# Optimization experiments

Measured on AMD Instinct MI355X. Metric: run time of the kernel, lower is better.

## Reference

```python
import jax, jax.numpy as jnp
import numpy as np

B, NPG, DEG, F, H, C = 256, 256, 16, 128, 128, 10
N = B * NPG
E = N * DEG
RATIO = 0.5
K1 = int(np.ceil(RATIO * NPG))       # 128
K2 = int(np.ceil(RATIO * K1))        # 64
K3 = int(np.ceil(RATIO * K2))        # 32


def _glorot(key, shape):
    lim = np.sqrt(6.0 / (shape[0] + shape[1]))
    return jax.random.uniform(key, shape, jnp.float32, -lim, lim)


def setup_inputs() -> dict:
    key = jax.random.key(0)
    ks = jax.random.split(key, 16)
    x = jax.random.normal(ks[0], (N, F), jnp.float32)
    epg = E // B
    g = jnp.repeat(jnp.arange(B, dtype=jnp.int32), epg)
    src = jax.random.randint(ks[1], (E,), 0, NPG, jnp.int32) + g * NPG
    dst = jax.random.randint(ks[2], (E,), 0, NPG, jnp.int32) + g * NPG
    edge_index = jnp.stack([src, dst])
    batch = jnp.repeat(jnp.arange(B, dtype=jnp.int32), NPG)
    return {
        "x": x, "edge_index": edge_index, "batch": batch,
        "W1": _glorot(ks[3], (F, H)), "b1": jnp.zeros((H,), jnp.float32),
        "Wp1": _glorot(ks[4], (H, 1)), "bp1": jnp.zeros((1,), jnp.float32),
        "W2": _glorot(ks[5], (H, H)), "b2": jnp.zeros((H,), jnp.float32),
        "Wp2": _glorot(ks[6], (H, 1)), "bp2": jnp.zeros((1,), jnp.float32),
        "W3": _glorot(ks[7], (H, H)), "b3": jnp.zeros((H,), jnp.float32),
        "Wp3": _glorot(ks[8], (H, 1)), "bp3": jnp.zeros((1,), jnp.float32),
        "Wl1": _glorot(ks[9], (2 * H, H)), "bl1": jnp.zeros((H,), jnp.float32),
        "Wl2": _glorot(ks[10], (H, H // 2)), "bl2": jnp.zeros((H // 2,), jnp.float32),
        "Wl3": _glorot(ks[11], (H // 2, C)), "bl3": jnp.zeros((C,), jnp.float32),
    }


def gcn_conv(x, src, dst, emask, nmask, W, b):
    # PyG GCNConv: symmetric normalization with self-loops, edge weights = emask.
    h = x @ W
    deg = jax.ops.segment_sum(emask, dst, num_segments=N) + nmask  # self-loop on active nodes
    dinv = jnp.where(deg > 0, jax.lax.rsqrt(deg), 0.0)
    w = emask * dinv[src] * dinv[dst]                      # [E]
    agg = jax.ops.segment_sum(h[src] * w[:, None], dst, num_segments=N)
    out = agg + h * (dinv * dinv * nmask)[:, None] + b
    return out * nmask[:, None]


def topk_pool(x, src, dst, emask, nmask, Wp, bp, k):
    # SAGPool-style gcn_pool: score via GCNConv(H->1), per-graph top-k,
    # x <- x * tanh(score) on kept nodes, edges restricted to kept nodes.
    s = gcn_conv(x, src, dst, emask, nmask, Wp, bp)[:, 0]   # [N]
    sm = jnp.where(nmask > 0, s, -jnp.inf).reshape(B, NPG)
    idx = jax.lax.top_k(sm, k)[1]                           # [B,k]
    newmask = jnp.zeros((B, NPG), x.dtype).at[jnp.arange(B)[:, None], idx].set(1.0).reshape(-1)
    x_new = x * jnp.tanh(s)[:, None] * newmask[:, None]
    emask_new = emask * newmask[src] * newmask[dst]
    return x_new, emask_new, newmask


def readout(x, nmask, batch):
    # cat([global_max_pool, global_mean_pool]) over remaining nodes per graph
    cnt = jax.ops.segment_sum(nmask, batch, num_segments=B)
    mean = jax.ops.segment_sum(x, batch, num_segments=B) / cnt[:, None]
    xinf = jnp.where(nmask[:, None] > 0, x, -jnp.inf)
    mx = jax.ops.segment_max(xinf, batch, num_segments=B)
    return jnp.concatenate([mx, mean], axis=1)


def reference(x, edge_index, batch, W1, b1, Wp1, bp1, W2, b2, Wp2, bp2, W3, b3, Wp3, bp3,
              Wl1, bl1, Wl2, bl2, Wl3, bl3):
    src, dst = edge_index[0], edge_index[1]
    emask = jnp.ones((E,), x.dtype)
    nmask = jnp.ones((N,), x.dtype)

    h = jax.nn.relu(gcn_conv(x, src, dst, emask, nmask, W1, b1))
    h, emask, nmask = topk_pool(h, src, dst, emask, nmask, Wp1, bp1, K1)
    x1 = readout(h, nmask, batch)

    h = jax.nn.relu(gcn_conv(h, src, dst, emask, nmask, W2, b2))
    h, emask, nmask = topk_pool(h, src, dst, emask, nmask, Wp2, bp2, K2)
    x2 = readout(h, nmask, batch)

    h = jax.nn.relu(gcn_conv(h, src, dst, emask, nmask, W3, b3))
    h, emask, nmask = topk_pool(h, src, dst, emask, nmask, Wp3, bp3, K3)
    x3 = readout(h, nmask, batch)

    z = x1 + x2 + x3
    z = jax.nn.relu(z @ Wl1 + bl1)   # dropout is identity in eval mode
    z = jax.nn.relu(z @ Wl2 + bl2)
    return jax.nn.log_softmax(z @ Wl3 + bl3, axis=-1)
```

## Files before the change

kernel.cpp:

```cpp
#include <hip/hip_runtime.h>
#include <math.h>

#define NB   256
#define NPG  256
#define NN   (NB * NPG)
#define NE   (NN * 16)
#define EPG  (NE / NB)
#define FD   128
#define NC   10
#define NSL  32
#define NEG_INF (-3.402823466e38f)

struct SM {
    float hs[NPG][FD];
    int   rp[NPG + 4];
    float nmloc[NPG];
    float dvv[NPG];
    float sw[NPG];
    float sf[NPG];
    float svv[NPG];
    float th[NPG];
    float zacc[2 * FD];
    int   si[NPG];
    int   kept[NPG];
    int   anode[NPG];
    float red_mx[16][FD];
    float red_sm[16][FD];
    unsigned char colb[EPG];
};

__device__ __forceinline__ float4& hsq(SM& sm, int v, int q) {
    return *(float4*)&sm.hs[v][(q ^ (v & 7)) << 2];
}

template <int NACT>
__device__ __forceinline__ void do_level(SM& sm,
                                         const float* __restrict__ Wmat,
                                         const float* __restrict__ bias,
                                         const float* __restrict__ Wp,
                                         const float* __restrict__ bpp,
                                         int tid) {
    constexpr int NPS = NACT / NSL;
    constexpr int K   = NACT / 2;
    constexpr int TPN = 1024 / NACT;
    const int f4 = tid & 31;
    const int s  = tid >> 5;

    {
        const int n = tid >> 2, sub = tid & 3;
        float part = 0.f;
        const float nmn = sm.nmloc[n];
        if (nmn > 0.f) {
            const int e1 = sm.rp[n + 1];
            for (int e = sm.rp[n] + sub; e < e1; e += 4)
                part += sm.nmloc[sm.colb[e]];
        }
        part += __shfl_xor(part, 1);
        part += __shfl_xor(part, 2);
        if (sub == 0)
            sm.dvv[n] = (nmn > 0.f) ? rsqrtf(1.f + part) : 0.f;
    }

    {
        int vr[NPS];
        float4 acc[NPS];
#pragma unroll
        for (int c = 0; c < NPS; ++c) {
            vr[c] = sm.anode[c * NSL + s];
            acc[c] = make_float4(0.f, 0.f, 0.f, 0.f);
        }
#pragma unroll 2
        for (int kq = 0; kq < 32; ++kq) {
            const int k0 = kq << 2;
            float4 w0 = *(const float4*)&Wmat[(k0 + 0) * FD + 4 * f4];
            float4 w1 = *(const float4*)&Wmat[(k0 + 1) * FD + 4 * f4];
            float4 w2 = *(const float4*)&Wmat[(k0 + 2) * FD + 4 * f4];
            float4 w3 = *(const float4*)&Wmat[(k0 + 3) * FD + 4 * f4];
#pragma unroll
            for (int c = 0; c < NPS; ++c) {
                float4 hv = hsq(sm, vr[c], kq);
                acc[c].x += hv.x * w0.x + hv.y * w1.x + hv.z * w2.x + hv.w * w3.x;
                acc[c].y += hv.x * w0.y + hv.y * w1.y + hv.z * w2.y + hv.w * w3.y;
                acc[c].z += hv.x * w0.z + hv.y * w1.z + hv.z * w2.z + hv.w * w3.z;
                acc[c].w += hv.x * w0.w + hv.y * w1.w + hv.z * w2.w + hv.w * w3.w;
            }
        }
#pragma unroll
        for (int c = 0; c < NPS; ++c)
            hsq(sm, vr[c], f4) = acc[c];
    }
    __syncthreads();

    const float4 b4  = *(const float4*)&bias[4 * f4];
    const float4 wp4 = *(const float4*)&Wp[4 * f4];
    float4 hreg[NPS];
#pragma unroll
    for (int c = 0; c < NPS; ++c) {
        const int v = sm.anode[c * NSL + s];
        const float dv_ = sm.dvv[v], dv2 = dv_ * dv_;
        const float4 hv = hsq(sm, v, f4);
        float4 acc;
        acc.x = hv.x * dv2 + b4.x;
        acc.y = hv.y * dv2 + b4.y;
        acc.z = hv.z * dv2 + b4.z;
        acc.w = hv.w * dv2 + b4.w;
        const int e0 = sm.rp[v], e1 = sm.rp[v + 1];
        int e = e0;
        for (; e + 4 <= e1; e += 4) {
            int u0 = sm.colb[e],     u1 = sm.colb[e + 1];
            int u2 = sm.colb[e + 2], u3 = sm.colb[e + 3];
            float w0 = sm.dvv[u0] * dv_, w1 = sm.dvv[u1] * dv_;
            float w2 = sm.dvv[u2] * dv_, w3 = sm.dvv[u3] * dv_;
            float4 h0 = hsq(sm, u0, f4);
            float4 h1 = hsq(sm, u1, f4);
            float4 h2 = hsq(sm, u2, f4);
            float4 h3 = hsq(sm, u3, f4);
            acc.x += w0 * h0.x + w1 * h1.x + w2 * h2.x + w3 * h3.x;
            acc.y += w0 * h0.y + w1 * h1.y + w2 * h2.y + w3 * h3.y;
            acc.z += w0 * h0.z + w1 * h1.z + w2 * h2.z + w3 * h3.z;
            acc.w += w0 * h0.w + w1 * h1.w + w2 * h2.w + w3 * h3.w;
        }
        for (; e < e1; ++e) {
            int u = sm.colb[e];
            float w = sm.dvv[u] * dv_;
            float4 hu = hsq(sm, u, f4);
            acc.x += w * hu.x; acc.y += w * hu.y;
            acc.z += w * hu.z; acc.w += w * hu.w;
        }
        acc.x = fmaxf(acc.x, 0.f);
        acc.y = fmaxf(acc.y, 0.f);
        acc.z = fmaxf(acc.z, 0.f);
        acc.w = fmaxf(acc.w, 0.f);
        hreg[c] = acc;
        float p = acc.x * wp4.x + acc.y * wp4.y + acc.z * wp4.z + acc.w * wp4.w;
        p += __shfl_xor(p, 1);
        p += __shfl_xor(p, 2);
        p += __shfl_xor(p, 4);
        p += __shfl_xor(p, 8);
        p += __shfl_xor(p, 16);
        if (f4 == 0) sm.sw[v] = p;
    }
    __syncthreads();

    {
        const int i = tid / TPN, sub = tid % TPN;
        const int v = sm.anode[i];
        const float dv_ = sm.dvv[v];
        float part = 0.f;
        const int e1 = sm.rp[v + 1];
        for (int e = sm.rp[v] + sub; e < e1; e += TPN) {
            int u = sm.colb[e];
            part += sm.dvv[u] * sm.sw[u];
        }
#pragma unroll
        for (int o = 1; o < TPN; o <<= 1) part += __shfl_xor(part, o);
        if (sub == 0) {
            float acc = sm.sw[v] * dv_ * dv_ + bpp[0] + dv_ * part;
            sm.sf[v] = acc;
            sm.svv[i] = acc;
        }
    }
    __syncthreads();

    float v_ = 0.f;
    int   id_ = 0;
    if (tid < NACT) { v_ = sm.svv[tid]; id_ = sm.anode[tid]; }
#pragma unroll
    for (int k = 2; k <= NACT; k <<= 1) {
#pragma unroll
        for (int j = k >> 1; j > 0; j >>= 1) {
            if (j < 64) {
                if (tid < NACT) {
                    float vp = __shfl_xor(v_, j);
                    int  idp = __shfl_xor(id_, j);
                    bool up    = ((tid & k) == 0);
                    bool lower = ((tid & j) == 0);
                    bool g = (v_ > vp) || (v_ == vp && id_ < idp);
                    if (g != (lower == up)) { v_ = vp; id_ = idp; }
                }
            } else {
                if (tid < NACT) { sm.svv[tid] = v_; sm.si[tid] = id_; }
                __syncthreads();
                if (tid < NACT) {
                    int p = tid ^ j;
                    float vp = sm.svv[p];
                    int  idp = sm.si[p];
                    bool up    = ((tid & k) == 0);
                    bool lower = ((tid & j) == 0);
                    bool g = (v_ > vp) || (v_ == vp && id_ < idp);
                    if (g != (lower == up)) { v_ = vp; id_ = idp; }
                }
                __syncthreads();
            }
        }
    }
    if (tid < NPG) sm.kept[tid] = 0;
    __syncthreads();
    if (tid < K) {
        sm.kept[id_] = 1;
        sm.th[id_] = tanhf(sm.sf[id_]);
    }
    __syncthreads();

    float4 mx4 = make_float4(NEG_INF, NEG_INF, NEG_INF, NEG_INF);
    float4 sm4 = make_float4(0.f, 0.f, 0.f, 0.f);
#pragma unroll
    for (int c = 0; c < NPS; ++c) {
        const int v = sm.anode[c * NSL + s];
        if (sm.kept[v]) {
            const float tg = sm.th[v];
            float4 val;
            val.x = hreg[c].x * tg;
            val.y = hreg[c].y * tg;
            val.z = hreg[c].z * tg;
            val.w = hreg[c].w * tg;
            hsq(sm, v, f4) = val;
            mx4.x = fmaxf(mx4.x, val.x); sm4.x += val.x;
            mx4.y = fmaxf(mx4.y, val.y); sm4.y += val.y;
            mx4.z = fmaxf(mx4.z, val.z); sm4.z += val.z;
            mx4.w = fmaxf(mx4.w, val.w); sm4.w += val.w;
        }
    }
    mx4.x = fmaxf(mx4.x, __shfl_xor(mx4.x, 32)); sm4.x += __shfl_xor(sm4.x, 32);
    mx4.y = fmaxf(mx4.y, __shfl_xor(mx4.y, 32)); sm4.y += __shfl_xor(sm4.y, 32);
    mx4.z = fmaxf(mx4.z, __shfl_xor(mx4.z, 32)); sm4.z += __shfl_xor(sm4.z, 32);
    mx4.w = fmaxf(mx4.w, __shfl_xor(mx4.w, 32)); sm4.w += __shfl_xor(sm4.w, 32);
    const int wv = tid >> 6;
    if ((tid & 63) < 32) {
        *(float4*)&sm.red_mx[wv][4 * f4] = mx4;
        *(float4*)&sm.red_sm[wv][4 * f4] = sm4;
    }
    __syncthreads();
    if (tid < FD) {
        float mx = NEG_INF, smv = 0.f;
#pragma unroll
        for (int i = 0; i < 16; ++i) {
            mx = fmaxf(mx, sm.red_mx[i][tid]);
            smv += sm.red_sm[i][tid];
        }
        sm.zacc[tid] += mx;
        sm.zacc[FD + tid] += smv / (float)K;
    }
    if (tid < NPG) sm.nmloc[tid] = (float)sm.kept[tid];
    if (tid < K) sm.anode[tid] = id_;
    __syncthreads();
}

__global__ __launch_bounds__(1024)
void k_mega(const float* __restrict__ x, const int* __restrict__ ei,
            const float* __restrict__ W1, const float* __restrict__ b1,
            const float* __restrict__ Wp1, const float* __restrict__ bp1,
            const float* __restrict__ W2, const float* __restrict__ b2,
            const float* __restrict__ Wp2, const float* __restrict__ bp2,
            const float* __restrict__ W3, const float* __restrict__ b3,
            const float* __restrict__ Wp3, const float* __restrict__ bp3,
            const float* __restrict__ Wl1, const float* __restrict__ bl1,
            const float* __restrict__ Wl2, const float* __restrict__ bl2,
            const float* __restrict__ Wl3, const float* __restrict__ bl3,
            float* __restrict__ out) {
    __shared__ SM sm;
    const int g = blockIdx.x, tid = threadIdx.x;
    const int gbase = g * NPG, ebase = g * EPG;
    const int* __restrict__ srcA = ei;
    const int* __restrict__ dstA = ei + NE;

    int myd[4], mys[4];
#pragma unroll
    for (int i = 0; i < 4; ++i) {
        int e = ebase + tid + i * 1024;
        myd[i] = dstA[e] - gbase;
        mys[i] = srcA[e] - gbase;
    }

    if (tid < NPG) sm.si[tid] = 0;
    __syncthreads();
#pragma unroll
    for (int i = 0; i < 4; ++i) atomicAdd(&sm.si[myd[i]], 1);
    __syncthreads();
    if (tid < NPG) sm.anode[tid] = sm.si[tid];
    __syncthreads();
    for (int o = 1; o < NPG; o <<= 1) {
        int add = 0;
        if (tid < NPG && tid >= o) add = sm.anode[tid - o];
        __syncthreads();
        if (tid < NPG) sm.anode[tid] += add;
        __syncthreads();
    }
    if (tid < NPG) {
        int excl = sm.anode[tid] - sm.si[tid];
        sm.rp[tid] = excl;
        sm.kept[tid] = excl;
        if (tid == 0) sm.rp[NPG] = EPG;
    }
    __syncthreads();
#pragma unroll
    for (int i = 0; i < 4; ++i) {
        int p = atomicAdd(&sm.kept[myd[i]], 1);
        sm.colb[p] = (unsigned char)mys[i];
    }

    {
        const int r0 = tid >> 5, f4 = tid & 31;
        for (int r = r0; r < NPG; r += NSL)
            hsq(sm, r, f4) =
                *(const float4*)&x[((size_t)(gbase + r)) * FD + 4 * f4];
    }
    if (tid < NPG) { sm.anode[tid] = tid; sm.nmloc[tid] = 1.f; }
    if (tid < 2 * FD) sm.zacc[tid] = 0.f;
    __syncthreads();

    do_level<256>(sm, W1, b1, Wp1, bp1, tid);
    do_level<128>(sm, W2, b2, Wp2, bp2, tid);
    do_level<64>(sm, W3, b3, Wp3, bp3, tid);

    if (tid < 128) {
        float a = bl1[tid];
#pragma unroll 8
        for (int k = 0; k < 256; ++k) a += sm.zacc[k] * Wl1[k * 128 + tid];
        sm.sw[tid] = fmaxf(a, 0.f);
    }
    __syncthreads();
    if (tid < 64) {
        float a = bl2[tid];
#pragma unroll 8
        for (int k = 0; k < 128; ++k) a += sm.sw[k] * Wl2[k * 64 + tid];
        sm.sf[tid] = fmaxf(a, 0.f);
    }
    __syncthreads();
    if (tid < NC) {
        float a = bl3[tid];
#pragma unroll
        for (int k = 0; k < 64; ++k) a += sm.sf[k] * Wl3[k * NC + tid];
        sm.svv[tid] = a;
    }
    __syncthreads();
    if (tid == 0) {
        float m = sm.svv[0];
        for (int c = 1; c < NC; ++c) m = fmaxf(m, sm.svv[c]);
        float se = 0.f;
        for (int c = 0; c < NC; ++c) se += expf(sm.svv[c] - m);
        float lse = m + logf(se);
        for (int c = 0; c < NC; ++c) out[g * NC + c] = sm.svv[c] - lse;
    }
}

extern "C" void kernel_launch(void* const* d_in, const int* in_sizes, int n_in,
                              void* d_out, int out_size, void* d_ws, size_t ws_size,
                              hipStream_t stream) {
    const float* x   = (const float*)d_in[0];
    const int*   ei  = (const int*)d_in[1];
    const float* W1  = (const float*)d_in[3];
    const float* b1  = (const float*)d_in[4];
    const float* Wp1 = (const float*)d_in[5];
    const float* bp1 = (const float*)d_in[6];
    const float* W2  = (const float*)d_in[7];
    const float* b2  = (const float*)d_in[8];
    const float* Wp2 = (const float*)d_in[9];
    const float* bp2 = (const float*)d_in[10];
    const float* W3  = (const float*)d_in[11];
    const float* b3  = (const float*)d_in[12];
    const float* Wp3 = (const float*)d_in[13];
    const float* bp3 = (const float*)d_in[14];
    const float* Wl1 = (const float*)d_in[15];
    const float* bl1 = (const float*)d_in[16];
    const float* Wl2 = (const float*)d_in[17];
    const float* bl2 = (const float*)d_in[18];
    const float* Wl3 = (const float*)d_in[19];
    const float* bl3 = (const float*)d_in[20];
    float* out = (float*)d_out;

    k_mega<<<NB, 1024, 0, stream>>>(x, ei,
                                    W1, b1, Wp1, bp1,
                                    W2, b2, Wp2, bp2,
                                    W3, b3, Wp3, bp3,
                                    Wl1, bl1, Wl2, bl2, Wl3, bl3, out);
}
```

Measured before the change: 127.0 us.

## Replace bitonic top-k with rank counting and retile transform and MLP head

Replaces the bitonic sort used for per-graph top-k, with its many barriers, by packing each score and node id into a 64-bit key and computing ranks through all-pairs counting. The kept list is then compacted in ascending node order with ballot and popcount. The feature transform now gives each active thread 8 nodes, so only NACT/8 row groups work and the other threads sit idle. The final MLP layers split each dot product across 4 or 8 lanes and combine them with shuffles. The intent is to cut synchronisation and serial loop depth, at the cost of more redundant compare work and lower thread utilisation in the matmul.

```diff
diff --git a/kernel.cpp b/kernel.cpp
--- a/kernel.cpp
+++ b/kernel.cpp
@@ -43,8 +43,10 @@
     constexpr int NPS = NACT / NSL;
     constexpr int K   = NACT / 2;
     constexpr int TPN = 1024 / NACT;
+    constexpr int SG  = NACT / 8;
     const int f4 = tid & 31;
     const int s  = tid >> 5;
+    unsigned long long* keys = (unsigned long long*)&sm.red_mx[0][0];
 
     {
         const int n = tid >> 2, sub = tid & 3;
@@ -61,12 +63,12 @@
             sm.dvv[n] = (nmn > 0.f) ? rsqrtf(1.f + part) : 0.f;
     }
 
-    {
-        int vr[NPS];
-        float4 acc[NPS];
-#pragma unroll
-        for (int c = 0; c < NPS; ++c) {
-            vr[c] = sm.anode[c * NSL + s];
+    if (s < SG) {
+        int vr[8];
+        float4 acc[8];
+#pragma unroll
+        for (int c = 0; c < 8; ++c) {
+            vr[c] = sm.anode[c * SG + s];
             acc[c] = make_float4(0.f, 0.f, 0.f, 0.f);
         }
 #pragma unroll 2
@@ -77,7 +79,7 @@
             float4 w2 = *(const float4*)&Wmat[(k0 + 2) * FD + 4 * f4];
             float4 w3 = *(const float4*)&Wmat[(k0 + 3) * FD + 4 * f4];
 #pragma unroll
-            for (int c = 0; c < NPS; ++c) {
+            for (int c = 0; c < 8; ++c) {
                 float4 hv = hsq(sm, vr[c], kq);
                 acc[c].x += hv.x * w0.x + hv.y * w1.x + hv.z * w2.x + hv.w * w3.x;
                 acc[c].y += hv.x * w0.y + hv.y * w1.y + hv.z * w2.y + hv.w * w3.y;
@@ -86,7 +88,7 @@
             }
         }
 #pragma unroll
-        for (int c = 0; c < NPS; ++c)
+        for (int c = 0; c < 8; ++c)
             hsq(sm, vr[c], f4) = acc[c];
     }
     __syncthreads();
@@ -157,48 +159,27 @@
         if (sub == 0) {
             float acc = sm.sw[v] * dv_ * dv_ + bpp[0] + dv_ * part;
             sm.sf[v] = acc;
-            sm.svv[i] = acc;
-        }
-    }
-    __syncthreads();
-
-    float v_ = 0.f;
-    int   id_ = 0;
-    if (tid < NACT) { v_ = sm.svv[tid]; id_ = sm.anode[tid]; }
-#pragma unroll
-    for (int k = 2; k <= NACT; k <<= 1) {
-#pragma unroll
-        for (int j = k >> 1; j > 0; j >>= 1) {
-            if (j < 64) {
-                if (tid < NACT) {
-                    float vp = __shfl_xor(v_, j);
-                    int  idp = __shfl_xor(id_, j);
-                    bool up    = ((tid & k) == 0);
-                    bool lower = ((tid & j) == 0);
-                    bool g = (v_ > vp) || (v_ == vp && id_ < idp);
-                    if (g != (lower == up)) { v_ = vp; id_ = idp; }
-                }
-            } else {
-                if (tid < NACT) { sm.svv[tid] = v_; sm.si[tid] = id_; }
-                __syncthreads();
-                if (tid < NACT) {
-                    int p = tid ^ j;
-                    float vp = sm.svv[p];
-                    int  idp = sm.si[p];
-                    bool up    = ((tid & k) == 0);
-                    bool lower = ((tid & j) == 0);
-                    bool g = (v_ > vp) || (v_ == vp && id_ < idp);
-                    if (g != (lower == up)) { v_ = vp; id_ = idp; }
-                }
-                __syncthreads();
-            }
-        }
-    }
-    if (tid < NPG) sm.kept[tid] = 0;
-    __syncthreads();
-    if (tid < K) {
-        sm.kept[id_] = 1;
-        sm.th[id_] = tanhf(sm.sf[id_]);
+            unsigned su = __float_as_uint(acc);
+            unsigned ou = (su & 0x80000000u) ? ~su : (su | 0x80000000u);
+            keys[i] = ((unsigned long long)(~ou) << 32) | (unsigned)v;
+        }
+        if (tid < NPG) sm.kept[tid] = 0;
+    }
+    __syncthreads();
+
+    {
+        const int i = tid / TPN, sub = tid % TPN;
+        const unsigned long long ki = keys[i];
+        int cnt = 0;
+        for (int t = sub; t < NACT; t += TPN)
+            cnt += (keys[t] < ki) ? 1 : 0;
+#pragma unroll
+        for (int o = 1; o < TPN; o <<= 1) cnt += __shfl_xor(cnt, o);
+        if (sub == 0 && cnt < K) {
+            int v = (int)(ki & 0xFFu);
+            sm.kept[v] = 1;
+            sm.th[v] = tanhf(sm.sf[v]);
+        }
     }
     __syncthreads();
 
@@ -231,6 +212,10 @@
         *(float4*)&sm.red_sm[wv][4 * f4] = sm4;
     }
     __syncthreads();
+
+    bool kp = (tid < NPG) && (sm.kept[tid] != 0);
+    unsigned long long mask = __ballot(kp);
+    if (tid < NPG && (tid & 63) == 0) sm.si[tid >> 6] = (int)__popcll(mask);
     if (tid < FD) {
         float mx = NEG_INF, smv = 0.f;
 #pragma unroll
@@ -241,8 +226,15 @@
         sm.zacc[tid] += mx;
         sm.zacc[FD + tid] += smv / (float)K;
     }
-    if (tid < NPG) sm.nmloc[tid] = (float)sm.kept[tid];
-    if (tid < K) sm.anode[tid] = id_;
+    __syncthreads();
+
+    if (tid < NPG) {
+        const int wvi = tid >> 6, lane = tid & 63;
+        int base = 0;
+        for (int w = 0; w < wvi; ++w) base += sm.si[w];
+        if (kp) sm.anode[base + (int)__popcll(mask & ((1ull << lane) - 1ull))] = tid;
+        sm.nmloc[tid] = kp ? 1.f : 0.f;
+    }
     __syncthreads();
 }
 
@@ -313,25 +305,38 @@
     do_level<128>(sm, W2, b2, Wp2, bp2, tid);
     do_level<64>(sm, W3, b3, Wp3, bp3, tid);
 
-    if (tid < 128) {
-        float a = bl1[tid];
-#pragma unroll 8
-        for (int k = 0; k < 256; ++k) a += sm.zacc[k] * Wl1[k * 128 + tid];
-        sm.sw[tid] = fmaxf(a, 0.f);
-    }
-    __syncthreads();
-    if (tid < 64) {
-        float a = bl2[tid];
-#pragma unroll 8
-        for (int k = 0; k < 128; ++k) a += sm.sw[k] * Wl2[k * 64 + tid];
-        sm.sf[tid] = fmaxf(a, 0.f);
-    }
-    __syncthreads();
-    if (tid < NC) {
-        float a = bl3[tid];
-#pragma unroll
-        for (int k = 0; k < 64; ++k) a += sm.sf[k] * Wl3[k * NC + tid];
-        sm.svv[tid] = a;
+    {
+        const int o = tid >> 2, sub = tid & 3;
+        if (tid < 512) {
+            float a = 0.f;
+            for (int k = sub; k < 256; k += 4) a += sm.zacc[k] * Wl1[k * 128 + o];
+            a += __shfl_xor(a, 1);
+            a += __shfl_xor(a, 2);
+            if (sub == 0) sm.sw[o] = fmaxf(a + bl1[o], 0.f);
+        }
+    }
+    __syncthreads();
+    {
+        const int o = tid >> 2, sub = tid & 3;
+        if (tid < 256) {
+            float a = 0.f;
+            for (int k = sub; k < 128; k += 4) a += sm.sw[k] * Wl2[k * 64 + o];
+            a += __shfl_xor(a, 1);
+            a += __shfl_xor(a, 2);
+            if (sub == 0) sm.sf[o] = fmaxf(a + bl2[o], 0.f);
+        }
+    }
+    __syncthreads();
+    {
+        const int o = tid >> 3, sub = tid & 7;
+        if (tid < 8 * NC) {
+            float a = 0.f;
+            for (int k = sub; k < 64; k += 8) a += sm.sf[k] * Wl3[k * NC + o];
+            a += __shfl_xor(a, 1);
+            a += __shfl_xor(a, 2);
+            a += __shfl_xor(a, 4);
+            if (sub == 0) sm.svv[o] = a + bl3[o];
+        }
     }
     __syncthreads();
     if (tid == 0) {
```

After: 142.6 us. 1.12x slower.
